# Optimization experiments

Hardware: AMD Instinct MI355X
Metric: run time of the kernel (lower is better)

The kernel has to match this reference:

```python
import jax, jax.numpy as jnp
import numpy as np

B, L, D, P = 8, 2048, 1024, 4  # batch, length, word_dim, phrase_len


def setup_inputs() -> dict:
    key = jax.random.key(0)
    kx, kw, kb = jax.random.split(key, 3)
    x = jax.random.normal(kx, (B, L, D), dtype=jnp.float32)
    # torch nn.Linear(phrase_dim, word_dim): W [out=D, in=D*P], b [D]
    scale = 1.0 / np.sqrt(D * P)
    W = jax.random.uniform(kw, (D, D * P), dtype=jnp.float32, minval=-scale, maxval=scale)
    b = jax.random.uniform(kb, (D,), dtype=jnp.float32, minval=-scale, maxval=scale)
    return {"x": x, "W": W, "b": b}


def reference(x, W, b):
    Bs, Ls, Ds = x.shape
    Ps = W.shape[1] // Ds  # phrase_len
    # gram[i][:, t] = x[:, t - i] (zero for t < i): left-pad by i, keep first L steps.
    # Stack on the LAST axis then reshape, matching torch's contiguous view over
    # (dim, phrase_len) -> feature index d*P + i.
    grams = jnp.stack(
        [jnp.pad(x, ((0, 0), (i, 0), (0, 0)))[:, :Ls, :] for i in range(Ps)],
        axis=-1,
    )  # [B, L, D, P]
    feat = grams.reshape(Bs, Ls, Ds * Ps)  # [B, L, D*P]
    # nn.Linear: y = feat @ W.T + b
    return jnp.einsum("blf,df->bld", feat, W) + b
```

## Files before the change

kernel.cpp:

```cpp
#include <hip/hip_runtime.h>
#include <hip/hip_bf16.h>
#include <stdint.h>

#define Bq 8
#define Lq 2048
#define Dq 1024
#define Pq 4
#define Kq 4096
#define LPAD 2056
#define BM 256
#define BN 256
#define BK 64

typedef __attribute__((ext_vector_type(8))) short short8;
typedef __attribute__((ext_vector_type(4))) float f32x4;

__device__ __forceinline__ unsigned short f2bf(float f) {
  unsigned u = __float_as_uint(f);
  u += 0x7FFFu + ((u >> 16) & 1u);
  return (unsigned short)(u >> 16);
}

__device__ __forceinline__ void gload_lds16(const void* g, void* l) {
  __builtin_amdgcn_global_load_lds(
      (const __attribute__((address_space(1))) void*)g,
      (__attribute__((address_space(3))) void*)l, 16, 0, 0);
}

__global__ void k_prep(const float* __restrict__ x, const float* __restrict__ W,
                       unsigned short* __restrict__ xp, unsigned short* __restrict__ Wp) {
  if (blockIdx.x < 8224u) {
    unsigned g = blockIdx.x * blockDim.x + threadIdx.x;
    unsigned base = g * 8;
    const unsigned total = (unsigned)Bq * LPAD * Dq;
    if (base >= total) return;
    unsigned t = base >> 10;
    unsigned b = t / LPAD;
    unsigned r = t - b * LPAD;
    unsigned d = base & 1023;
    short8 o;
    if (r >= 3 && r < 3 + Lq) {
      const float* s = x + ((size_t)b * Lq + (r - 3)) * Dq + d;
      float4 v0 = *(const float4*)(s);
      float4 v1 = *(const float4*)(s + 4);
      o[0] = (short)f2bf(v0.x); o[1] = (short)f2bf(v0.y);
      o[2] = (short)f2bf(v0.z); o[3] = (short)f2bf(v0.w);
      o[4] = (short)f2bf(v1.x); o[5] = (short)f2bf(v1.y);
      o[6] = (short)f2bf(v1.z); o[7] = (short)f2bf(v1.w);
    } else {
      o = (short8)0;
    }
    *(short8*)(xp + base) = o;
  } else {
    unsigned g = (blockIdx.x - 8224u) * blockDim.x + threadIdx.x;
    unsigned base = g * 8;
    unsigned d = base >> 12;
    unsigned rem = base & 4095;
    unsigned dp = rem >> 2;
    const float4* src = (const float4*)(W + base);
    float4 v0 = src[0];
    float4 v1 = src[1];
    float a0[4] = {v0.x, v0.y, v0.z, v0.w};
    float a1[4] = {v1.x, v1.y, v1.z, v1.w};
#pragma unroll
    for (int i = 0; i < 4; ++i) {
      unsigned packed = (unsigned)f2bf(a0[i]) | ((unsigned)f2bf(a1[i]) << 16);
      *(unsigned*)(Wp + (size_t)d * 4096 + (size_t)i * 1024 + dp) = packed;
    }
  }
}


#define VM6 asm volatile("s_waitcnt vmcnt(6)" ::: "memory")
#define VM4 asm volatile("s_waitcnt vmcnt(4)" ::: "memory")
#define VM0 asm volatile("s_waitcnt vmcnt(0)" ::: "memory")
#define BAR __builtin_amdgcn_s_barrier()

#define STAGE_A(buf, kt, h) do { \
    const unsigned scl_ = ((((unsigned)(bRow0 + (h) * 64 - ((kt) >> 4))) << 10) + (((unsigned)(kt) & 15u) << 6)) << 1; \
    _Pragma("unroll") for (int q_ = 0; q_ < 2; ++q_) \
      gload_lds16((const char*)xp + (thrA[q_] + scl_), \
                  lds + ((buf) << 15) + ((h) << 14) + (q_ << 13) + (tid << 4)); \
  } while (0)

#define STAGE_B(buf, kt, h) do { \
    const unsigned scl_ = ((((unsigned)(n0 + (h) * 32)) << 12) + ((unsigned)(kt) << 6)) << 1; \
    _Pragma("unroll") for (int q_ = 0; q_ < 2; ++q_) \
      gload_lds16((const char*)Wp + (thrB[q_] + scl_), \
                  lds + 65536 + ((buf) << 15) + ((h) << 14) + (q_ << 13) + (tid << 4)); \
  } while (0)

#define READ_A(dst, buf, h) do { \
    _Pragma("unroll") for (int mi = 0; mi < 4; ++mi) \
    _Pragma("unroll") for (int kk = 0; kk < 2; ++kk) \
      dst[mi][kk] = *(const short8*)(lds + (((buf) << 15) + ((h) << 14)) + aRC[mi][kk]); \
  } while (0)

#define READ_B(dst, buf, h) do { \
    _Pragma("unroll") for (int ni = 0; ni < 2; ++ni) \
    _Pragma("unroll") for (int kk = 0; kk < 2; ++kk) \
      dst[ni][kk] = *(const short8*)(lds + (((buf) << 15) + ((h) << 14)) + bRC[ni][kk]); \
  } while (0)

#define MFMAQ(mh, nh, A, Bv) do { \
    __builtin_amdgcn_s_setprio(1); \
    _Pragma("unroll") for (int mi = 0; mi < 4; ++mi) \
    _Pragma("unroll") for (int ni = 0; ni < 2; ++ni) \
    _Pragma("unroll") for (int kk = 0; kk < 2; ++kk) \
      acc[(mh) * 4 + mi][(nh) * 2 + ni] = __builtin_amdgcn_mfma_f32_16x16x32_bf16( \
          A[mi][kk], Bv[ni][kk], acc[(mh) * 4 + mi][(nh) * 2 + ni], 0, 0, 0); \
    __builtin_amdgcn_s_setprio(0); \
  } while (0)

__global__ void __launch_bounds__(512, 2)
k_gemm(const unsigned short* __restrict__ xp,
       const unsigned short* __restrict__ Wp,
       const float* __restrict__ bias,
       float* __restrict__ out) {
  __shared__ __attribute__((aligned(16))) unsigned char lds[131072];

  const int tid  = threadIdx.x;
  const int lane = tid & 63;
  const int w    = tid >> 6;
  const int wm   = w >> 2;
  const int wn   = w & 3;

  const int bid = blockIdx.x;
  const int swz = (bid & 7) * 32 + (bid >> 3);
  const int m0 = (swz >> 2) * BM;
  const int n0 = (swz & 3) * BN;
  const int b  = m0 >> 11;
  const int l0 = m0 & 2047;
  const int bRow0 = b * LPAD + l0 + 3;

  const int sr0 = tid >> 3;
  const unsigned clog = ((unsigned)((tid & 7) ^ (sr0 & 7))) << 3;
  unsigned thrA[2], thrB[2];
  const unsigned nb0 = (((unsigned)sr0 >> 5) << 6) + ((unsigned)sr0 & 31);
#pragma unroll
  for (int q = 0; q < 2; ++q) {
    thrA[q] = ((((unsigned)(sr0 + q * 128)) << 10) + clog) << 1;
    thrB[q] = (((nb0 + q * 128u) << 12) + clog) << 1;
  }

  int aRC[4][2], bRC[2][2];
  {
    int colByte[2];
#pragma unroll
    for (int kk = 0; kk < 2; ++kk)
      colByte[kk] = (kk * 64 + ((lane >> 4) << 4)) ^ ((lane & 7) << 4);
#pragma unroll
    for (int mi = 0; mi < 4; ++mi)
#pragma unroll
      for (int kk = 0; kk < 2; ++kk)
        aRC[mi][kk] = ((wm * 64 + mi * 16 + (lane & 15)) << 7) + colByte[kk];
#pragma unroll
    for (int ni = 0; ni < 2; ++ni)
#pragma unroll
      for (int kk = 0; kk < 2; ++kk)
        bRC[ni][kk] = 65536 + ((wn * 32 + ni * 16 + (lane & 15)) << 7) + colByte[kk];
  }

  f32x4 acc[8][4] = {};
  short8 fa[4][2], bX[2][2], bY[2][2];

  STAGE_A(0, 0, 0);
  STAGE_B(0, 0, 1);
  STAGE_A(0, 0, 1);
  STAGE_B(0, 0, 0);
  VM4;
  STAGE_A(1, 1, 0);
  STAGE_B(1, 1, 1);
  STAGE_A(1, 1, 1);
  VM6;
  BAR;

#pragma unroll 1
  for (int it = 0; it < 31; ++it) {
    const int T = it * 2;
    READ_A(fa, 0, 0); READ_B(bX, 0, 0); READ_B(bY, 0, 1);
    STAGE_B(1, T + 1, 0);
    BAR; MFMAQ(0, 0, fa, bX); BAR;
    STAGE_A(0, T + 2, 0);
    BAR; MFMAQ(0, 1, fa, bY); BAR;
    READ_A(fa, 0, 1);
    STAGE_B(0, T + 2, 1);
    BAR; MFMAQ(1, 1, fa, bY); BAR;
    STAGE_A(0, T + 2, 1);
    VM6;
    BAR; MFMAQ(1, 0, fa, bX); BAR;
    READ_A(fa, 1, 0); READ_B(bX, 1, 0); READ_B(bY, 1, 1);
    STAGE_B(0, T + 2, 0);
    BAR; MFMAQ(0, 0, fa, bX); BAR;
    STAGE_A(1, T + 3, 0);
    BAR; MFMAQ(0, 1, fa, bY); BAR;
    READ_A(fa, 1, 1);
    STAGE_B(1, T + 3, 1);
    BAR; MFMAQ(1, 1, fa, bY); BAR;
    STAGE_A(1, T + 3, 1);
    VM6;
    BAR; MFMAQ(1, 0, fa, bX); BAR;
  }

  READ_A(fa, 0, 0); READ_B(bX, 0, 0); READ_B(bY, 0, 1);
  STAGE_B(1, 63, 0);
  BAR; MFMAQ(0, 0, fa, bX); BAR;
  MFMAQ(0, 1, fa, bY);
  READ_A(fa, 0, 1);
  MFMAQ(1, 1, fa, bY);
  MFMAQ(1, 0, fa, bX);
  VM0;
  BAR;
  READ_A(fa, 1, 0); READ_B(bX, 1, 0); READ_B(bY, 1, 1);
  MFMAQ(0, 0, fa, bX);
  MFMAQ(0, 1, fa, bY);
  READ_A(fa, 1, 1);
  MFMAQ(1, 1, fa, bY);
  MFMAQ(1, 0, fa, bX);

#pragma unroll
  for (int nig = 0; nig < 4; ++nig) {
    const int col = n0 + wn * 64 + nig * 16 + (lane & 15);
    const float bv = bias[col];
#pragma unroll
    for (int mig = 0; mig < 8; ++mig) {
      const int row0 = m0 + wm * 128 + mig * 16 + ((lane >> 4) << 2);
#pragma unroll
      for (int t2 = 0; t2 < 4; ++t2)
        out[(size_t)(row0 + t2) * Dq + col] = acc[mig][nig][t2] + bv;
    }
  }
}

__global__ void k_naive(const float* __restrict__ x, const float* __restrict__ W,
                        const float* __restrict__ bias, float* __restrict__ out) {
  size_t g = (size_t)blockIdx.x * blockDim.x + threadIdx.x;
  const size_t total = (size_t)Bq * Lq * Dq;
  if (g >= total) return;
  int d = (int)(g & 1023);
  int l = (int)((g >> 10) & 2047);
  int b = (int)(g >> 21);
  float s = bias[d];
  for (int i = 0; i < Pq; ++i) {
    if (l - i < 0) continue;
    const float* xr = x + ((size_t)b * Lq + (l - i)) * Dq;
    const float* wr = W + (size_t)d * Kq + i;
    float accv = 0.f;
    for (int dp = 0; dp < Dq; ++dp) accv += xr[dp] * wr[(size_t)dp * 4];
    s += accv;
  }
  out[g] = s;
}

extern "C" void kernel_launch(void* const* d_in, const int* in_sizes, int n_in,
                              void* d_out, int out_size, void* d_ws, size_t ws_size,
                              hipStream_t stream) {
  const float* x    = (const float*)d_in[0];
  const float* W    = (const float*)d_in[1];
  const float* bias = (const float*)d_in[2];
  float* out = (float*)d_out;

  const size_t WP_BYTES = (size_t)Dq * Kq * sizeof(unsigned short);
  const size_t XP_BYTES = (size_t)Bq * LPAD * Dq * sizeof(unsigned short);

  if (ws_size < WP_BYTES + XP_BYTES) {
    const size_t total = (size_t)Bq * Lq * Dq;
    k_naive<<<(unsigned)((total + 255) / 256), 256, 0, stream>>>(x, W, bias, out);
    return;
  }

  unsigned short* Wp = (unsigned short*)d_ws;
  unsigned short* xp = (unsigned short*)((char*)d_ws + WP_BYTES);

  k_prep<<<10272, 256, 0, stream>>>(x, W, xp, Wp);
  k_gemm<<<dim3((Bq * Lq / BM) * (Dq / BN)), 512, 0, stream>>>(xp, Wp, bias, out);
}
```

Measured before the change: 133.1 us.

## Restructure GEMM main loop into fewer barriers with coarser MFMA batches

Replaces the eight MFMA quarter-blocks per iteration, each bracketed by two barriers, with four larger MFMA batches that each cover both N halves, and one barrier per batch. Global-to-LDS staging is reordered so that several tiles are issued together, and the vmcnt waits change to 8, with 2 in the tail. The aim is to cut barrier and synchronisation overhead and keep the MFMA pipe busier. The cost is more tightly coupled buffer reuse timing, which could cause LDS hazards if the wait counts are wrong.

```diff
diff --git a/kernel.cpp b/kernel.cpp
--- a/kernel.cpp
+++ b/kernel.cpp
@@ -71,10 +71,11 @@
 }
 
 
-#define VM6 asm volatile("s_waitcnt vmcnt(6)" ::: "memory")
-#define VM4 asm volatile("s_waitcnt vmcnt(4)" ::: "memory")
+#define VM8 asm volatile("s_waitcnt vmcnt(8)" ::: "memory")
+#define VM2 asm volatile("s_waitcnt vmcnt(2)" ::: "memory")
 #define VM0 asm volatile("s_waitcnt vmcnt(0)" ::: "memory")
 #define BAR __builtin_amdgcn_s_barrier()
+#define NOPS ((void)0)
 
 #define STAGE_A(buf, kt, h) do { \
     const unsigned scl_ = ((((unsigned)(bRow0 + (h) * 64 - ((kt) >> 4))) << 10) + (((unsigned)(kt) & 15u) << 6)) << 1; \
@@ -102,13 +103,18 @@
       dst[ni][kk] = *(const short8*)(lds + (((buf) << 15) + ((h) << 14)) + bRC[ni][kk]); \
   } while (0)
 
-#define MFMAQ(mh, nh, A, Bv) do { \
+#define MFMA_PAIR(mh) do { \
     __builtin_amdgcn_s_setprio(1); \
-    _Pragma("unroll") for (int mi = 0; mi < 4; ++mi) \
-    _Pragma("unroll") for (int ni = 0; ni < 2; ++ni) \
-    _Pragma("unroll") for (int kk = 0; kk < 2; ++kk) \
-      acc[(mh) * 4 + mi][(nh) * 2 + ni] = __builtin_amdgcn_mfma_f32_16x16x32_bf16( \
-          A[mi][kk], Bv[ni][kk], acc[(mh) * 4 + mi][(nh) * 2 + ni], 0, 0, 0); \
+    _Pragma("unroll") for (int kk = 0; kk < 2; ++kk) { \
+      _Pragma("unroll") for (int mi = 0; mi < 4; ++mi) \
+      _Pragma("unroll") for (int ni = 0; ni < 2; ++ni) \
+        acc[(mh) * 4 + mi][ni] = __builtin_amdgcn_mfma_f32_16x16x32_bf16( \
+            fa[mi][kk], bX[ni][kk], acc[(mh) * 4 + mi][ni], 0, 0, 0); \
+      _Pragma("unroll") for (int mi = 0; mi < 4; ++mi) \
+      _Pragma("unroll") for (int ni = 0; ni < 2; ++ni) \
+        acc[(mh) * 4 + mi][2 + ni] = __builtin_amdgcn_mfma_f32_16x16x32_bf16( \
+            fa[mi][kk], bY[ni][kk], acc[(mh) * 4 + mi][2 + ni], 0, 0, 0); \
+    } \
     __builtin_amdgcn_s_setprio(0); \
   } while (0)
 
@@ -165,58 +171,55 @@
   short8 fa[4][2], bX[2][2], bY[2][2];
 
   STAGE_A(0, 0, 0);
+  STAGE_B(0, 0, 0);
   STAGE_B(0, 0, 1);
   STAGE_A(0, 0, 1);
-  STAGE_B(0, 0, 0);
-  VM4;
   STAGE_A(1, 1, 0);
+  STAGE_B(1, 1, 0);
   STAGE_B(1, 1, 1);
-  STAGE_A(1, 1, 1);
-  VM6;
+  VM8;
   BAR;
 
 #pragma unroll 1
   for (int it = 0; it < 31; ++it) {
     const int T = it * 2;
     READ_A(fa, 0, 0); READ_B(bX, 0, 0); READ_B(bY, 0, 1);
-    STAGE_B(1, T + 1, 0);
-    BAR; MFMAQ(0, 0, fa, bX); BAR;
-    STAGE_A(0, T + 2, 0);
-    BAR; MFMAQ(0, 1, fa, bY); BAR;
+    STAGE_A(1, T + 1, 1);
+    MFMA_PAIR(0);
+    VM8;
+    BAR;
     READ_A(fa, 0, 1);
-    STAGE_B(0, T + 2, 1);
-    BAR; MFMAQ(1, 1, fa, bY); BAR;
+    STAGE_A(0, T + 2, 0); STAGE_B(0, T + 2, 0); STAGE_B(0, T + 2, 1);
+    MFMA_PAIR(1);
+    VM8;
+    BAR;
+    READ_A(fa, 1, 0); READ_B(bX, 1, 0); READ_B(bY, 1, 1);
     STAGE_A(0, T + 2, 1);
-    VM6;
-    BAR; MFMAQ(1, 0, fa, bX); BAR;
-    READ_A(fa, 1, 0); READ_B(bX, 1, 0); READ_B(bY, 1, 1);
-    STAGE_B(0, T + 2, 0);
-    BAR; MFMAQ(0, 0, fa, bX); BAR;
-    STAGE_A(1, T + 3, 0);
-    BAR; MFMAQ(0, 1, fa, bY); BAR;
+    MFMA_PAIR(0);
+    VM8;
+    BAR;
     READ_A(fa, 1, 1);
-    STAGE_B(1, T + 3, 1);
-    BAR; MFMAQ(1, 1, fa, bY); BAR;
-    STAGE_A(1, T + 3, 1);
-    VM6;
-    BAR; MFMAQ(1, 0, fa, bX); BAR;
+    STAGE_A(1, T + 3, 0); STAGE_B(1, T + 3, 0); STAGE_B(1, T + 3, 1);
+    MFMA_PAIR(1);
+    VM8;
+    BAR;
   }
 
   READ_A(fa, 0, 0); READ_B(bX, 0, 0); READ_B(bY, 0, 1);
-  STAGE_B(1, 63, 0);
-  BAR; MFMAQ(0, 0, fa, bX); BAR;
-  MFMAQ(0, 1, fa, bY);
+  STAGE_A(1, 63, 1);
+  MFMA_PAIR(0);
+  VM8;
+  BAR;
   READ_A(fa, 0, 1);
-  MFMAQ(1, 1, fa, bY);
-  MFMAQ(1, 0, fa, bX);
+  MFMA_PAIR(1);
+  VM2;
+  BAR;
+  READ_A(fa, 1, 0); READ_B(bX, 1, 0); READ_B(bY, 1, 1);
+  MFMA_PAIR(0);
   VM0;
   BAR;
-  READ_A(fa, 1, 0); READ_B(bX, 1, 0); READ_B(bY, 1, 1);
-  MFMAQ(0, 0, fa, bX);
-  MFMAQ(0, 1, fa, bY);
   READ_A(fa, 1, 1);
-  MFMAQ(1, 1, fa, bY);
-  MFMAQ(1, 0, fa, bX);
+  MFMA_PAIR(1);
 
 #pragma unroll
   for (int nig = 0; nig < 4; ++nig) {
```

Result: faster. 129.0 us (-3.1%).
